# Kernel optimization log

Hardware: AMD Instinct MI355X
Metric: run time of the kernel (lower is better)

The kernel has to match this reference:

```python
import jax, jax.numpy as jnp
import numpy as np

B, N, F_IN = 32, 1024, 64   # batch, num_nodes, diffusion_size[0]
K = 3                        # expansion_step
H = 2                        # num_heads
HID, RAW, OUT, CLS = 128, 128, 128, 2
D1, D2 = 128, 128            # diffusion_size[1], diffusion_size[2]
CAT = D1 + RAW               # concat dim fed to attention (h || h_prime) = 256


def setup_inputs() -> dict:
    key = jax.random.key(0)
    ks = jax.random.split(key, 40)
    g = lambda i, shape: jax.random.normal(ks[i], shape, dtype=jnp.float32) * 0.05
    inp = {
        'X': jax.random.normal(ks[0], (B, N, F_IN), dtype=jnp.float32),
        'A': jax.random.uniform(ks[1], (B, N, N), dtype=jnp.float32),
        # transition tensors / mixing weights (only the 2 layers used in forward)
        'T': g(2, (2, K, N, N)),
        'theta': jnp.full((2, K), 1.0 / K, dtype=jnp.float32),
        # raw feature projection
        'W_raw': g(3, (F_IN, RAW)), 'b_raw': jnp.zeros((RAW,), jnp.float32),
        # diffusion layer linears
        'Wd0': g(4, (F_IN, D1)), 'bd0': jnp.zeros((D1,), jnp.float32),
        'Wd1': g(5, (D1, D2)),   'bd1': jnp.zeros((D2,), jnp.float32),
        # final classifier
        'W_fin': g(6, (OUT, CLS)), 'b_fin': jnp.zeros((CLS,), jnp.float32),
    }
    # two CatMultiAttn blocks: q/k/v projections (CAT->HID), out proj (HID->OUT)
    i = 7
    for l in range(2):
        for nm in ('q', 'k', 'v'):
            inp[f'W{nm}{l}'] = g(i, (CAT, HID)); i += 1
            inp[f'b{nm}{l}'] = jnp.zeros((HID,), jnp.float32)
        inp[f'Wo{l}'] = g(i, (HID, OUT)); i += 1
        inp[f'bo{l}'] = jnp.zeros((OUT,), jnp.float32)
    return inp


def _diffusion(theta_l, T_l, h, A, W, b):
    # Q = sum_k theta_k * T_k  (generalized graph diffusion transition)
    Q = jnp.einsum('k,kij->ij', theta_l, T_l)          # [N,N]
    S = Q[None, :, :] * A                               # [B,N,N] mask by adjacency
    z = jnp.einsum('bij,bjf->bif', S, h)                # diffuse features
    return jax.nn.relu(z @ W + b)


def _cat_attn(h, hp, Wq, bq, Wk, bk, Wv, bv, Wo, bo):
    # concatenate diffused + embedding features, multi-head self-attn over nodes
    x = jnp.concatenate([h, hp], axis=-1)               # [B,N,CAT]
    b, n, _ = x.shape
    q = (x @ Wq + bq).reshape(b, n, H, HID // H)
    k = (x @ Wk + bk).reshape(b, n, H, HID // H)
    v = (x @ Wv + bv).reshape(b, n, H, HID // H)
    scale = jnp.asarray(1.0 / np.sqrt(HID // H), x.dtype)
    s = jnp.einsum('bnhd,bmhd->bhnm', q, k) * scale     # [B,H,N,N]
    p = jax.nn.softmax(s, axis=-1)
    ctx = jnp.einsum('bhnm,bmhd->bnhd', p, v).reshape(b, n, HID)
    return jax.nn.relu(ctx @ Wo + bo)


def reference(X, A, T, theta, W_raw, b_raw, Wd0, bd0, Wd1, bd1,
              W_fin, b_fin,
              Wq0, bq0, Wk0, bk0, Wv0, bv0, Wo0, bo0,
              Wq1, bq1, Wk1, bk1, Wv1, bv1, Wo1, bo1):
    theta_soft = jax.nn.softmax(theta, axis=-1)         # [2,K]
    h_prime = X @ W_raw + b_raw                          # [B,N,RAW]
    # layer 0
    h = _diffusion(theta_soft[0], T[0], X, A, Wd0, bd0)  # [B,N,D1]
    h_prime = _cat_attn(h, h_prime, Wq0, bq0, Wk0, bk0, Wv0, bv0, Wo0, bo0)
    # layer 1 (residual fusion)
    h = _diffusion(theta_soft[1], T[1], h, A, Wd1, bd1)  # [B,N,D2]
    h_prime = h_prime + _cat_attn(h, h_prime, Wq1, bq1, Wk1, bk1, Wv1, bv1, Wo1, bo1)
    return h_prime @ W_fin + b_fin                       # [B,N,CLS]
```

## Files before the change

kernel.cpp:

```cpp
#include <hip/hip_runtime.h>
#include <hip/hip_bf16.h>

typedef __hip_bfloat16 bf16;
typedef __attribute__((ext_vector_type(8))) short s8b;
typedef __attribute__((ext_vector_type(4))) short s4b;
typedef __attribute__((ext_vector_type(4))) float f4;

#define BB   32
#define NN   1024
#define FIN  64
#define HEADS 2
#define DH   64
#define HIDD 128
#define SZQ  ((size_t)BB * NN * HIDD)

__device__ __forceinline__ ushort f2bf(float x) {
    bf16 h = __float2bfloat16(x);
    return *(ushort*)&h;
}
__device__ __forceinline__ float bfbits2f(ushort h) {
    union { uint u; float f; } c; c.u = (uint)h << 16; return c.f;
}
__device__ __forceinline__ uint pk_bf16(float lo, float hi) {
    return (uint)f2bf(lo) | ((uint)f2bf(hi) << 16);
}
union U8 { short s[8]; s8b v; };
union U4 { short s[4]; s4b v; };
union UQ { ushort u[8]; s8b v; };

__global__ __launch_bounds__(256) void setup_kernel(
        const float* __restrict__ raw, const float* __restrict__ d0,
        const float* __restrict__ d1,
        const float* __restrict__ q0w, const float* __restrict__ k0w,
        const float* __restrict__ v0w, const float* __restrict__ o0w,
        const float* __restrict__ q1w, const float* __restrict__ k1w,
        const float* __restrict__ v1w, const float* __restrict__ o1w,
        ushort* __restrict__ Whi, ushort* __restrict__ Wlo,
        const float* __restrict__ T, const float* __restrict__ theta,
        ushort* __restrict__ Q0hi, ushort* __restrict__ Q0lo,
        ushort* __restrict__ Q1hi, ushort* __restrict__ Q1lo,
        const float* __restrict__ X,
        ushort* __restrict__ XT_hi, ushort* __restrict__ XT_lo) {
    __shared__ float tile[64][65];
    const int bid = blockIdx.x;
    const int t = threadIdx.x;
    if (bid < 1024) {
        int id = bid * 256 + t;
        const float* src; int K, off;
        if      (id <   8192) { src = raw; K =  64; off = 0; }
        else if (id <  16384) { src = d0;  K =  64; off = 8192; }
        else if (id <  32768) { src = d1;  K = 128; off = 16384; }
        else if (id <  65536) { src = q0w; K = 256; off = 32768; }
        else if (id <  98304) { src = k0w; K = 256; off = 65536; }
        else if (id < 131072) { src = v0w; K = 256; off = 98304; }
        else if (id < 147456) { src = o0w; K = 128; off = 131072; }
        else if (id < 180224) { src = q1w; K = 256; off = 147456; }
        else if (id < 212992) { src = k1w; K = 256; off = 180224; }
        else if (id < 245760) { src = v1w; K = 256; off = 212992; }
        else                  { src = o1w; K = 128; off = 245760; }
        int il = id - off;
        int k = il >> 7, c = il & 127;
        float w = src[il];
        ushort h = f2bf(w);
        Whi[off + c * K + k] = h;
        Wlo[off + c * K + k] = f2bf(w - bfbits2f(h));
    } else if (bid < 1536) {
        const int tb = bid - 1024;
        const int b  = tb >> 4;
        const int n0 = (tb & 15) * 64;
        {
            int nl = t >> 2, f0 = (t & 3) * 16;
            const float* xp = X + ((size_t)b * NN + n0 + nl) * 64 + f0;
#pragma unroll
            for (int i = 0; i < 16; i += 4)
                *(float4*)&tile[nl][f0 + i] = *(const float4*)(xp + i);
        }
        __syncthreads();
        {
            int f = t >> 2, n1 = (t & 3) * 16;
            U8 h0, h1, l0, l1;
#pragma unroll
            for (int i = 0; i < 16; i++) {
                float v = tile[n1 + i][f];
                ushort hh = f2bf(v);
                ushort ll = f2bf(v - bfbits2f(hh));
                if (i < 8) { h0.s[i] = (short)hh; l0.s[i] = (short)ll; }
                else       { h1.s[i - 8] = (short)hh; l1.s[i - 8] = (short)ll; }
            }
            size_t gb = ((size_t)b * 64 + f) * NN + n0 + n1;
            *(s8b*)&XT_hi[gb]     = h0.v;  *(s8b*)&XT_hi[gb + 8] = h1.v;
            *(s8b*)&XT_lo[gb]     = l0.v;  *(s8b*)&XT_lo[gb + 8] = l1.v;
        }
    } else {
        const int layer = (bid < 2048) ? 0 : 1;
        ushort* Qhi = layer ? Q1hi : Q0hi;
        ushort* Qlo = layer ? Q1lo : Q0lo;
        float t0 = theta[layer * 3 + 0];
        float t1 = theta[layer * 3 + 1];
        float t2 = theta[layer * 3 + 2];
        float m  = fmaxf(t0, fmaxf(t1, t2));
        float e0 = expf(t0 - m), e1 = expf(t1 - m), e2 = expf(t2 - m);
        float inv = 1.0f / (e0 + e1 + e2);
        e0 *= inv; e1 *= inv; e2 *= inv;
        size_t base = ((size_t)((bid - 1536) & 511) * 256 + t) * 8;
        const float* Tl = T + (size_t)layer * 3 * NN * NN;
        U8 hi, lo;
#pragma unroll
        for (int i = 0; i < 8; i++) {
            float q = e0 * Tl[base + i]
                    + e1 * Tl[base + i + (size_t)NN * NN]
                    + e2 * Tl[base + i + (size_t)2 * NN * NN];
            ushort hh = f2bf(q);
            hi.s[i] = (short)hh;
            lo.s[i] = (short)f2bf(q - bfbits2f(hh));
        }
        *(s8b*)&Qhi[base] = hi.v;
        *(s8b*)&Qlo[base] = lo.v;
    }
}

template<int F, bool WRITE_HT>
__global__ __launch_bounds__(512, 4) void diff_dense_kernel(
        const ushort* __restrict__ Qhi, const ushort* __restrict__ Qlo,
        const float* __restrict__ A,
        const ushort* __restrict__ hT_hi, const ushort* __restrict__ hT_lo,
        const ushort* __restrict__ WT_hi, const ushort* __restrict__ WT_lo,
        const float* __restrict__ bias,
        float* __restrict__ hout,
        ushort* __restrict__ hiT, ushort* __restrict__ loT) {
    constexpr int SS  = 72;
    constexpr int NT  = F / 16;
    constexpr int NCW = NT / 4;
    constexpr int SZ2 = F + 8;
    constexpr int P1 = 2 * 64 * SS + 2 * F * SS;
    constexpr int P2 = 2 * 64 * SZ2 + 2 * 128 * 40;
    __shared__ short smem[(P1 > P2) ? P1 : P2];
    short* Shi = smem;
    short* Slo = Shi + 64 * SS;
    short* Hhi = Slo + 64 * SS;
    short* Hlo = Hhi + (size_t)F * SS;
    short* Zhi = smem;
    short* Zlo = Zhi + 64 * SZ2;
    short* Wsh = Zlo + 64 * SZ2;
    short* Wsl = Wsh + 128 * 40;

    const int bidx = blockIdx.x;
    const int u  = bidx >> 3;
    const int b  = (bidx & 7) + 8 * (u >> 4);
    const int i0 = (u & 15) * 64;
    const int t  = threadIdx.x;
    const int w  = t >> 6, lane = t & 63;
    const int quad = lane >> 4, c = lane & 15;
    const int rh = w >> 2;
    const int ch = w & 3;

    const int srow = t >> 3, scol = (t & 7) * 8;
    const float*  Ap = A   + ((size_t)b * NN + i0 + srow) * NN + scol;
    const ushort* Qh = Qhi + (size_t)(i0 + srow) * NN + scol;
    const ushort* Ql = Qlo + (size_t)(i0 + srow) * NN + scol;
    constexpr int HTR = 512 / F;
    constexpr int HJ  = 64 / HTR;
    constexpr int HV  = HJ / 8;
    const int hrow = t / HTR, hcol = (t % HTR) * HJ;
    const ushort* Hh = hT_hi + ((size_t)b * F + hrow) * NN + hcol;
    const ushort* Hl = hT_lo + ((size_t)b * F + hrow) * NN + hcol;

    f4 acc[2][NCW];
#pragma unroll
    for (int st = 0; st < 2; st++)
#pragma unroll
        for (int i = 0; i < NCW; i++) acc[st][i] = (f4){0.f, 0.f, 0.f, 0.f};

    float4 a0 = *(const float4*)Ap, a1 = *(const float4*)(Ap + 4);
    s8b hhv[HV], hlv[HV];
#pragma unroll
    for (int vv = 0; vv < HV; vv++) {
        hhv[vv] = *(const s8b*)(Hh + 8 * vv);
        hlv[vv] = *(const s8b*)(Hl + 8 * vv);
    }
    UQ qh, ql;
    qh.v = *(const s8b*)Qh;
    ql.v = *(const s8b*)Ql;

#pragma unroll 1
    for (int j0 = 0; j0 < NN; j0 += 64) {
        __syncthreads();
        {
            float av[8] = {a0.x, a0.y, a0.z, a0.w, a1.x, a1.y, a1.z, a1.w};
            U8 hi, lo;
#pragma unroll
            for (int i = 0; i < 8; i++) {
                float q = bfbits2f(qh.u[i]) + bfbits2f(ql.u[i]);
                float s = q * av[i];
                ushort hb = f2bf(s);
                hi.s[i] = (short)hb;
                lo.s[i] = (short)f2bf(s - bfbits2f(hb));
            }
            *(s8b*)&Shi[srow * SS + scol] = hi.v;
            *(s8b*)&Slo[srow * SS + scol] = lo.v;
#pragma unroll
            for (int vv = 0; vv < HV; vv++) {
                *(s8b*)&Hhi[hrow * SS + hcol + 8 * vv] = hhv[vv];
                *(s8b*)&Hlo[hrow * SS + hcol + 8 * vv] = hlv[vv];
            }
        }
        __syncthreads();

        if (j0 + 64 < NN) {
            a0 = *(const float4*)(Ap + j0 + 64);
            a1 = *(const float4*)(Ap + j0 + 68);
#pragma unroll
            for (int vv = 0; vv < HV; vv++) {
                hhv[vv] = *(const s8b*)(Hh + j0 + 64 + 8 * vv);
                hlv[vv] = *(const s8b*)(Hl + j0 + 64 + 8 * vv);
            }
            qh.v = *(const s8b*)(Qh + j0 + 64);
            ql.v = *(const s8b*)(Ql + j0 + 64);
        }

#pragma unroll
        for (int ks = 0; ks < 2; ks++) {
            s8b ah0 = *(const s8b*)&Shi[(32 * rh + c) * SS + ks * 32 + quad * 8];
            s8b al0 = *(const s8b*)&Slo[(32 * rh + c) * SS + ks * 32 + quad * 8];
            s8b ah1 = *(const s8b*)&Shi[(32 * rh + 16 + c) * SS + ks * 32 + quad * 8];
            s8b al1 = *(const s8b*)&Slo[(32 * rh + 16 + c) * SS + ks * 32 + quad * 8];
#pragma unroll
            for (int ctn = 0; ctn < NCW; ctn++) {
                const int nt = ch * NCW + ctn;
                s8b bhi = *(const s8b*)&Hhi[(nt * 16 + c) * SS + ks * 32 + quad * 8];
                s8b blo = *(const s8b*)&Hlo[(nt * 16 + c) * SS + ks * 32 + quad * 8];
                acc[0][ctn] = __builtin_amdgcn_mfma_f32_16x16x32_bf16(ah0, bhi, acc[0][ctn], 0, 0, 0);
                acc[0][ctn] = __builtin_amdgcn_mfma_f32_16x16x32_bf16(al0, bhi, acc[0][ctn], 0, 0, 0);
                acc[0][ctn] = __builtin_amdgcn_mfma_f32_16x16x32_bf16(ah0, blo, acc[0][ctn], 0, 0, 0);
                acc[1][ctn] = __builtin_amdgcn_mfma_f32_16x16x32_bf16(ah1, bhi, acc[1][ctn], 0, 0, 0);
                acc[1][ctn] = __builtin_amdgcn_mfma_f32_16x16x32_bf16(al1, bhi, acc[1][ctn], 0, 0, 0);
                acc[1][ctn] = __builtin_amdgcn_mfma_f32_16x16x32_bf16(ah1, blo, acc[1][ctn], 0, 0, 0);
            }
        }
    }

    __syncthreads();
#pragma unroll
    for (int st = 0; st < 2; st++)
#pragma unroll
        for (int ctn = 0; ctn < NCW; ctn++)
#pragma unroll
            for (int r = 0; r < 4; r++) {
                const int row = 32 * rh + 16 * st + quad * 4 + r;
                const int col = (ch * NCW + ctn) * 16 + c;
                float v = acc[st][ctn][r];
                ushort hh = f2bf(v);
                Zhi[row * SZ2 + col] = (short)hh;
                Zlo[row * SZ2 + col] = (short)f2bf(v - bfbits2f(hh));
            }

    const int rh2 = w >> 2;
    const int ch2 = w & 3;
    f4 acc2[2][2];
#pragma unroll
    for (int st = 0; st < 2; st++)
#pragma unroll
        for (int i = 0; i < 2; i++) acc2[st][i] = (f4){0.f, 0.f, 0.f, 0.f};

    constexpr int NKT = F / 32;
    const int wcc = t >> 2, wkk = (t & 3) * 8;
    s8b pwh = *(const s8b*)&WT_hi[(size_t)wcc * F + wkk];
    s8b pwl = *(const s8b*)&WT_lo[(size_t)wcc * F + wkk];
    for (int kt = 0; kt < NKT; kt++) {
        __syncthreads();
        *(s8b*)&Wsh[wcc * 40 + wkk] = pwh;
        *(s8b*)&Wsl[wcc * 40 + wkk] = pwl;
        __syncthreads();
        if (kt + 1 < NKT) {
            size_t gsrc = (size_t)wcc * F + (kt + 1) * 32 + wkk;
            pwh = *(const s8b*)&WT_hi[gsrc];
            pwl = *(const s8b*)&WT_lo[gsrc];
        }

        s8b ah0 = *(const s8b*)&Zhi[(32 * rh2 + c) * SZ2 + kt * 32 + quad * 8];
        s8b al0 = *(const s8b*)&Zlo[(32 * rh2 + c) * SZ2 + kt * 32 + quad * 8];
        s8b ah1 = *(const s8b*)&Zhi[(32 * rh2 + 16 + c) * SZ2 + kt * 32 + quad * 8];
        s8b al1 = *(const s8b*)&Zlo[(32 * rh2 + 16 + c) * SZ2 + kt * 32 + quad * 8];
#pragma unroll
        for (int ct = 0; ct < 2; ct++) {
            s8b bh = *(const s8b*)&Wsh[(ch2 * 32 + ct * 16 + c) * 40 + quad * 8];
            s8b bl = *(const s8b*)&Wsl[(ch2 * 32 + ct * 16 + c) * 40 + quad * 8];
            acc2[0][ct] = __builtin_amdgcn_mfma_f32_16x16x32_bf16(ah0, bh, acc2[0][ct], 0, 0, 0);
            acc2[0][ct] = __builtin_amdgcn_mfma_f32_16x16x32_bf16(al0, bh, acc2[0][ct], 0, 0, 0);
            acc2[0][ct] = __builtin_amdgcn_mfma_f32_16x16x32_bf16(ah0, bl, acc2[0][ct], 0, 0, 0);
            acc2[1][ct] = __builtin_amdgcn_mfma_f32_16x16x32_bf16(ah1, bh, acc2[1][ct], 0, 0, 0);
            acc2[1][ct] = __builtin_amdgcn_mfma_f32_16x16x32_bf16(al1, bh, acc2[1][ct], 0, 0, 0);
            acc2[1][ct] = __builtin_amdgcn_mfma_f32_16x16x32_bf16(ah1, bl, acc2[1][ct], 0, 0, 0);
        }
    }

#pragma unroll
    for (int st = 0; st < 2; st++) {
        const int rg0 = i0 + 32 * rh2 + 16 * st + quad * 4;
#pragma unroll
        for (int ct = 0; ct < 2; ct++) {
            const int col = ch2 * 32 + ct * 16 + c;
            float bv = bias[col];
            float vv[4];
#pragma unroll
            for (int r = 0; r < 4; r++) {
                float v = fmaxf(acc2[st][ct][r] + bv, 0.f);
                hout[((size_t)b * NN + rg0 + r) * 128 + col] = v;
                vv[r] = v;
            }
            if (WRITE_HT) {
                U4 ph, pl;
#pragma unroll
                for (int r = 0; r < 4; r++) {
                    ushort hh = f2bf(vv[r]);
                    ph.s[r] = (short)hh;
                    pl.s[r] = (short)f2bf(vv[r] - bfbits2f(hh));
                }
                size_t tb = ((size_t)b * 128 + col) * NN + rg0;
                *(s4b*)&hiT[tb] = ph.v;
                *(s4b*)&loT[tb] = pl.v;
            }
        }
    }
}

template<int K1, int K2, int CB, bool RELU, bool RESID, int OMODE>
__global__ __launch_bounds__(512) void dense_mfma_kernel(
        const float* __restrict__ in1, const float* __restrict__ in2,
        const ushort* __restrict__ WT_hi, const ushort* __restrict__ WT_lo,
        const float* __restrict__ bias, const float* __restrict__ biask,
        const float* __restrict__ biasv,
        float* __restrict__ out, ushort* __restrict__ outq) {
    constexpr int KD  = K1 + K2;
    constexpr int NKT = KD / 32;
    constexpr int NCH = CB / 32;
    constexpr int WCH = CB * 4;
    constexpr int WPT = (WCH + 511) / 512;
    __shared__ short Xhi[128][40], Xlo[128][40];
    __shared__ short Whi[CB][40], Wlo[CB][40];

    int bx, by;
    if (OMODE == 1) {
        const int xcd = blockIdx.x & 7, qq = blockIdx.x >> 3;
        by = qq & 1;
        bx = ((qq >> 1) << 3) | xcd;
    } else { bx = blockIdx.x; by = blockIdx.y; }
    const int r0 = bx * 128;
    const int c0 = by * CB;
    const int t  = threadIdx.x;
    const int w  = t >> 6, lane = t & 63;
    const int quad = lane >> 4, c = lane & 15;
    const int rh = w >> 1;
    const int ch = w & 1;

    f4 acc[2][NCH];
#pragma unroll
    for (int st = 0; st < 2; st++)
#pragma unroll
        for (int i = 0; i < NCH; i++) acc[st][i] = (f4){0.f, 0.f, 0.f, 0.f};

    const int xrow = t >> 2, xkk = (t & 3) * 8;
    float4 pa, pbq;
    s8b pwh[WPT], pwl[WPT];
    auto loadX = [&](int k0) {
        int g = r0 + xrow;
        const float* p;
        if (K2 > 0) {
            int k = k0 + xkk;
            p = (k < K1) ? (in1 + (size_t)g * K1 + k)
                         : (in2 + (size_t)g * K2 + (k - K1));
        } else {
            p = in1 + (size_t)g * K1 + k0 + xkk;
        }
        pa = *(const float4*)p; pbq = *(const float4*)(p + 4);
    };
    auto loadW = [&](int k0) {
#pragma unroll
        for (int i = 0; i < WPT; i++) {
            int id = t + i * 512;
            if ((WCH % 512 == 0) || id < WCH) {
                int cc = id >> 2, kk = (id & 3) * 8;
                size_t gsrc = (size_t)(c0 + cc) * KD + k0 + kk;
                pwh[i] = *(const s8b*)&WT_hi[gsrc];
                pwl[i] = *(const s8b*)&WT_lo[gsrc];
            }
        }
    };
    loadX(0); loadW(0);

    for (int kt = 0; kt < NKT; kt++) {
        __syncthreads();
        {
            float sv[8] = {pa.x, pa.y, pa.z, pa.w, pbq.x, pbq.y, pbq.z, pbq.w};
            U8 hi, lo;
#pragma unroll
            for (int i = 0; i < 8; i++) {
                ushort hh = f2bf(sv[i]);
                hi.s[i] = (short)hh;
                lo.s[i] = (short)f2bf(sv[i] - bfbits2f(hh));
            }
            *(s8b*)&Xhi[xrow][xkk] = hi.v;
            *(s8b*)&Xlo[xrow][xkk] = lo.v;
        }
        {
#pragma unroll
            for (int i = 0; i < WPT; i++) {
                int id = t + i * 512;
                if ((WCH % 512 == 0) || id < WCH) {
                    int cc = id >> 2, kk = (id & 3) * 8;
                    *(s8b*)&Whi[cc][kk] = pwh[i];
                    *(s8b*)&Wlo[cc][kk] = pwl[i];
                }
            }
        }
        __syncthreads();
        if (kt + 1 < NKT) { loadX(kt * 32 + 32); loadW(kt * 32 + 32); }

        s8b ah0 = *(const s8b*)&Xhi[32 * rh + c][quad * 8];
        s8b al0 = *(const s8b*)&Xlo[32 * rh + c][quad * 8];
        s8b ah1 = *(const s8b*)&Xhi[32 * rh + 16 + c][quad * 8];
        s8b al1 = *(const s8b*)&Xlo[32 * rh + 16 + c][quad * 8];
#pragma unroll
        for (int ct = 0; ct < NCH; ct++) {
            s8b bh = *(const s8b*)&Whi[ch * (CB / 2) + ct * 16 + c][quad * 8];
            s8b bl = *(const s8b*)&Wlo[ch * (CB / 2) + ct * 16 + c][quad * 8];
            acc[0][ct] = __builtin_amdgcn_mfma_f32_16x16x32_bf16(ah0, bh, acc[0][ct], 0, 0, 0);
            acc[0][ct] = __builtin_amdgcn_mfma_f32_16x16x32_bf16(al0, bh, acc[0][ct], 0, 0, 0);
            acc[0][ct] = __builtin_amdgcn_mfma_f32_16x16x32_bf16(ah0, bl, acc[0][ct], 0, 0, 0);
            acc[1][ct] = __builtin_amdgcn_mfma_f32_16x16x32_bf16(ah1, bh, acc[1][ct], 0, 0, 0);
            acc[1][ct] = __builtin_amdgcn_mfma_f32_16x16x32_bf16(al1, bh, acc[1][ct], 0, 0, 0);
            acc[1][ct] = __builtin_amdgcn_mfma_f32_16x16x32_bf16(ah1, bl, acc[1][ct], 0, 0, 0);
        }
    }

#pragma unroll
    for (int st = 0; st < 2; st++) {
        const int row_g0 = r0 + 32 * rh + 16 * st + quad * 4;
#pragma unroll
        for (int ct = 0; ct < NCH; ct++) {
            const int col = c0 + ch * (CB / 2) + ct * 16 + c;
            if (OMODE == 1) {
                int tensor = col >> 7, cc2 = col & 127;
                float bv = (tensor == 0 ? bias : tensor == 1 ? biask : biasv)[cc2];
                int head = cc2 >> 6, d = cc2 & 63;
                int b = row_g0 >> 10, n = row_g0 & 1023;
                if (tensor == 2) {
                    U4 pk;
#pragma unroll
                    for (int r = 0; r < 4; r++) pk.s[r] = (short)f2bf(acc[st][ct][r] + bv);
                    size_t addr = (((size_t)b * HEADS + head) * 64 + d) * NN + n;
                    *(s4b*)&outq[2 * SZQ + addr] = pk.v;
                } else {
                    ushort* dst = outq + (size_t)tensor * SZQ
                                + (((size_t)b * HEADS + head) * NN + n) * 64 + d;
#pragma unroll
                    for (int r = 0; r < 4; r++) dst[(size_t)r * 64] = f2bf(acc[st][ct][r] + bv);
                }
            } else {
                float bv = bias[col];
#pragma unroll
                for (int r = 0; r < 4; r++) {
                    float v = acc[st][ct][r] + bv;
                    if (RELU) v = fmaxf(v, 0.f);
                    size_t o = (size_t)(row_g0 + r) * 128 + col;
                    if (RESID) v += out[o];
                    out[o] = v;
                }
            }
        }
    }
}

template<bool FINAL>
__global__ __launch_bounds__(512) void attn_oproj_kernel(
        const ushort* __restrict__ q, const ushort* __restrict__ k,
        const ushort* __restrict__ vt,
        const ushort* __restrict__ WoT_hi, const ushort* __restrict__ WoT_lo,
        const float* __restrict__ bo,
        float* __restrict__ hp,
        const float* __restrict__ Wfin, const float* __restrict__ bfin,
        float* __restrict__ fout) {
    constexpr int ZS = 136;
    constexpr int PB = 2 * 128 * ZS + 2 * 128 * 40 + 512;
    __shared__ short smem[PB];
    short* Ks  = smem;
    short* Vt  = smem + 128 * 72;
    short* Zhi = smem;
    short* Zlo = Zhi + 128 * ZS;
    short* Wsh = Zlo + 128 * ZS;
    short* Wsl = Wsh + 128 * 40;
    float* red = (float*)(Wsl + 128 * 40);

    const int bidx = blockIdx.x;
    const int u  = bidx >> 3;
    const int b  = (bidx & 7) + 8 * (u >> 3);
    const int n0 = (u & 7) * 128;
    const int t  = threadIdx.x;
    const int w  = t >> 6;
    const int lane = t & 63;
    const int quad = lane >> 4, c = lane & 15;
    const float scale = 0.125f;

    const int skey = t >> 2, sd0 = (t & 3) * 16;
    const int svd  = t >> 3, svc = (t & 7) * 16;

    s8b pk0, pk1, pv0, pv1;
    auto loadKV = [&](size_t base, int kt0) {
        const ushort* kr = k + base + (size_t)(kt0 + skey) * 64 + sd0;
        pk0 = *(const s8b*)kr;
        pk1 = *(const s8b*)(kr + 8);
        const ushort* vr = vt + base + (size_t)svd * NN + kt0 + svc;
        pv0 = *(const s8b*)vr;
        pv1 = *(const s8b*)(vr + 8);
    };

    f4 Oh[2][4];
    float li[2];

#pragma unroll
    for (int h = 0; h < 2; h++) {
        const size_t kvbase = ((size_t)(b * HEADS + h)) * NN * 64;
        s8b qf0, qf1;
        {
            const ushort* qrow = q + kvbase + (size_t)(n0 + 16 * w + c) * 64;
            qf0 = *(const s8b*)(qrow + quad * 8);
            qf1 = *(const s8b*)(qrow + 32 + quad * 8);
        }
        if (h == 0) loadKV(kvbase, 0);
        f4 O[4];
#pragma unroll
        for (int i = 0; i < 4; i++) O[i] = (f4){0.f, 0.f, 0.f, 0.f};
        float l_i = 0.f;

        for (int kt0 = 0; kt0 < NN; kt0 += 128) {
            __syncthreads();
            {
                *(s8b*)&Ks[skey * 72 + sd0]     = pk0;
                *(s8b*)&Ks[skey * 72 + sd0 + 8] = pk1;
                *(s8b*)&Vt[svd * 136 + svc]     = pv0;
                *(s8b*)&Vt[svd * 136 + svc + 8] = pv1;
            }
            __syncthreads();
            if (kt0 + 128 < NN)      loadKV(kvbase, kt0 + 128);
            else if (h == 0)         loadKV(kvbase + (size_t)NN * 64, 0);

            f4 sg[4][2];
#pragma unroll
            for (int g = 0; g < 4; g++) {
                const int kb = g * 32;
                sg[g][0] = (f4){0.f, 0.f, 0.f, 0.f};
                sg[g][1] = (f4){0.f, 0.f, 0.f, 0.f};
#pragma unroll
                for (int ck = 0; ck < 2; ck++) {
                    s8b ka = *(const s8b*)&Ks[(kb + c) * 72 + ck * 32 + quad * 8];
                    s8b kB = *(const s8b*)&Ks[(kb + 16 + c) * 72 + ck * 32 + quad * 8];
                    s8b qf = ck ? qf1 : qf0;
                    sg[g][0] = __builtin_amdgcn_mfma_f32_16x16x32_bf16(ka, qf, sg[g][0], 0, 0, 0);
                    sg[g][1] = __builtin_amdgcn_mfma_f32_16x16x32_bf16(kB, qf, sg[g][1], 0, 0, 0);
                }
            }
            float pv[4][8];
            float ps = 0.f;
#pragma unroll
            for (int g = 0; g < 4; g++)
#pragma unroll
                for (int r = 0; r < 4; r++) {
                    pv[g][r]     = __expf(sg[g][0][r] * scale);
                    pv[g][4 + r] = __expf(sg[g][1][r] * scale);
                    ps += pv[g][r] + pv[g][4 + r];
                }
            ps += __shfl_xor(ps, 16);
            ps += __shfl_xor(ps, 32);
            l_i += ps;

            int addr0 = ((((2 * quad) & 3) << 4) | c) << 2;
            int addr1 = ((((2 * quad + 1) & 3) << 4) | c) << 2;
            int tsel = quad >> 1;
#pragma unroll
            for (int g = 0; g < 4; g++) {
                const int kb = g * 32;
                uint Da01 = pk_bf16(pv[g][0], pv[g][1]), Da23 = pk_bf16(pv[g][2], pv[g][3]);
                uint Db01 = pk_bf16(pv[g][4], pv[g][5]), Db23 = pk_bf16(pv[g][6], pv[g][7]);
                int A01_0 = __builtin_amdgcn_ds_bpermute(addr0, (int)Da01);
                int A23_0 = __builtin_amdgcn_ds_bpermute(addr0, (int)Da23);
                int B01_0 = __builtin_amdgcn_ds_bpermute(addr0, (int)Db01);
                int B23_0 = __builtin_amdgcn_ds_bpermute(addr0, (int)Db23);
                int A01_1 = __builtin_amdgcn_ds_bpermute(addr1, (int)Da01);
                int A23_1 = __builtin_amdgcn_ds_bpermute(addr1, (int)Da23);
                int B01_1 = __builtin_amdgcn_ds_bpermute(addr1, (int)Db01);
                int B23_1 = __builtin_amdgcn_ds_bpermute(addr1, (int)Db23);
                union { int i[4]; s8b s; } pf;
                pf.i[0] = tsel ? B01_0 : A01_0;
                pf.i[1] = tsel ? B23_0 : A23_0;
                pf.i[2] = tsel ? B01_1 : A01_1;
                pf.i[3] = tsel ? B23_1 : A23_1;
#pragma unroll
                for (int dt = 0; dt < 4; dt++) {
                    s8b vf = *(const s8b*)&Vt[(16 * dt + c) * 136 + kb + quad * 8];
                    O[dt] = __builtin_amdgcn_mfma_f32_16x16x32_bf16(vf, pf.s, O[dt], 0, 0, 0);
                }
            }
        }
        li[h] = 1.0f / l_i;
#pragma unroll
        for (int dt = 0; dt < 4; dt++) Oh[h][dt] = O[dt];
    }

    __syncthreads();
    {
        const int zrow = 16 * w + c;
#pragma unroll
        for (int h = 0; h < 2; h++) {
            float inv = li[h];
#pragma unroll
            for (int dt = 0; dt < 4; dt++) {
                U4 ph, pl;
#pragma unroll
                for (int r = 0; r < 4; r++) {
                    float v = Oh[h][dt][r] * inv;
                    ushort hh = f2bf(v);
                    ph.s[r] = (short)hh;
                    pl.s[r] = (short)f2bf(v - bfbits2f(hh));
                }
                int col = h * 64 + 16 * dt + 4 * quad;
                *(s4b*)&Zhi[zrow * ZS + col] = ph.v;
                *(s4b*)&Zlo[zrow * ZS + col] = pl.v;
            }
        }
    }

    const int rh = w >> 1;
    const int ch = w & 1;
    f4 acc[2][4];
#pragma unroll
    for (int st = 0; st < 2; st++)
#pragma unroll
        for (int i = 0; i < 4; i++) acc[st][i] = (f4){0.f, 0.f, 0.f, 0.f};

    const int occ = t >> 2, okk = (t & 3) * 8;
    s8b owh = *(const s8b*)&WoT_hi[(size_t)occ * 128 + okk];
    s8b owl = *(const s8b*)&WoT_lo[(size_t)occ * 128 + okk];
    for (int kt = 0; kt < 4; kt++) {
        __syncthreads();
        *(s8b*)&Wsh[occ * 40 + okk] = owh;
        *(s8b*)&Wsl[occ * 40 + okk] = owl;
        __syncthreads();
        if (kt + 1 < 4) {
            size_t gsrc = (size_t)occ * 128 + (kt + 1) * 32 + okk;
            owh = *(const s8b*)&WoT_hi[gsrc];
            owl = *(const s8b*)&WoT_lo[gsrc];
        }

        s8b ah0 = *(const s8b*)&Zhi[(32 * rh + c) * ZS + kt * 32 + quad * 8];
        s8b al0 = *(const s8b*)&Zlo[(32 * rh + c) * ZS + kt * 32 + quad * 8];
        s8b ah1 = *(const s8b*)&Zhi[(32 * rh + 16 + c) * ZS + kt * 32 + quad * 8];
        s8b al1 = *(const s8b*)&Zlo[(32 * rh + 16 + c) * ZS + kt * 32 + quad * 8];
#pragma unroll
        for (int ct = 0; ct < 4; ct++) {
            s8b bh = *(const s8b*)&Wsh[(ch * 64 + ct * 16 + c) * 40 + quad * 8];
            s8b bl = *(const s8b*)&Wsl[(ch * 64 + ct * 16 + c) * 40 + quad * 8];
            acc[0][ct] = __builtin_amdgcn_mfma_f32_16x16x32_bf16(ah0, bh, acc[0][ct], 0, 0, 0);
            acc[0][ct] = __builtin_amdgcn_mfma_f32_16x16x32_bf16(al0, bh, acc[0][ct], 0, 0, 0);
            acc[0][ct] = __builtin_amdgcn_mfma_f32_16x16x32_bf16(ah0, bl, acc[0][ct], 0, 0, 0);
            acc[1][ct] = __builtin_amdgcn_mfma_f32_16x16x32_bf16(ah1, bh, acc[1][ct], 0, 0, 0);
            acc[1][ct] = __builtin_amdgcn_mfma_f32_16x16x32_bf16(al1, bh, acc[1][ct], 0, 0, 0);
            acc[1][ct] = __builtin_amdgcn_mfma_f32_16x16x32_bf16(ah1, bl, acc[1][ct], 0, 0, 0);
        }
    }

    if (FINAL) {
        float fc[2][2][4];
#pragma unroll
        for (int st = 0; st < 2; st++)
#pragma unroll
            for (int o = 0; o < 2; o++)
#pragma unroll
                for (int r = 0; r < 4; r++) fc[st][o][r] = 0.f;
#pragma unroll
        for (int ct = 0; ct < 4; ct++) {
            const int col = ch * 64 + ct * 16 + c;
            float bv = bo[col];
            float w0 = Wfin[col * 2], w1 = Wfin[col * 2 + 1];
#pragma unroll
            for (int st = 0; st < 2; st++) {
                const size_t rg = (size_t)b * NN + n0 + 32 * rh + 16 * st + quad * 4;
#pragma unroll
                for (int r = 0; r < 4; r++) {
                    float v = fmaxf(acc[st][ct][r] + bv, 0.f);
                    v += hp[(rg + r) * 128 + col];
                    fc[st][0][r] += v * w0;
                    fc[st][1][r] += v * w1;
                }
            }
        }
#pragma unroll
        for (int st = 0; st < 2; st++)
#pragma unroll
            for (int r = 0; r < 4; r++) {
                float a0 = fc[st][0][r], a1 = fc[st][1][r];
#pragma unroll
                for (int off = 1; off < 16; off <<= 1) {
                    a0 += __shfl_xor(a0, off, 16);
                    a1 += __shfl_xor(a1, off, 16);
                }
                fc[st][0][r] = a0; fc[st][1][r] = a1;
            }
        if (ch == 1 && c == 0) {
#pragma unroll
            for (int st = 0; st < 2; st++)
#pragma unroll
                for (int r = 0; r < 4; r++) {
                    int lr = 32 * rh + 16 * st + quad * 4 + r;
                    red[lr * 2]     = fc[st][0][r];
                    red[lr * 2 + 1] = fc[st][1][r];
                }
        }
        __syncthreads();
        if (ch == 0 && c == 0) {
#pragma unroll
            for (int st = 0; st < 2; st++)
#pragma unroll
                for (int r = 0; r < 4; r++) {
                    int lr = 32 * rh + 16 * st + quad * 4 + r;
                    size_t row = (size_t)b * NN + n0 + lr;
                    fout[row * 2]     = fc[st][0][r] + red[lr * 2]     + bfin[0];
                    fout[row * 2 + 1] = fc[st][1][r] + red[lr * 2 + 1] + bfin[1];
                }
        }
        return;
    }

#pragma unroll
    for (int st = 0; st < 2; st++) {
        const size_t rg = (size_t)b * NN + n0 + 32 * rh + 16 * st + quad * 4;
#pragma unroll
        for (int ct = 0; ct < 4; ct++) {
            const int col = ch * 64 + ct * 16 + c;
            float bv = bo[col];
#pragma unroll
            for (int r = 0; r < 4; r++)
                hp[(rg + r) * 128 + col] = fmaxf(acc[st][ct][r] + bv, 0.f);
        }
    }
}

extern "C" void kernel_launch(void* const* d_in, const int* in_sizes, int n_in,
                              void* d_out, int out_size, void* d_ws, size_t ws_size,
                              hipStream_t stream) {
    (void)in_sizes; (void)n_in; (void)out_size; (void)ws_size;
    const float* X     = (const float*)d_in[0];
    const float* A     = (const float*)d_in[1];
    const float* T     = (const float*)d_in[2];
    const float* theta = (const float*)d_in[3];
    const float* W_raw = (const float*)d_in[4];
    const float* b_raw = (const float*)d_in[5];
    const float* Wd0   = (const float*)d_in[6];
    const float* bd0   = (const float*)d_in[7];
    const float* Wd1   = (const float*)d_in[8];
    const float* bd1   = (const float*)d_in[9];
    const float* W_fin = (const float*)d_in[10];
    const float* b_fin = (const float*)d_in[11];
    const float* Wq0 = (const float*)d_in[12]; const float* bq0 = (const float*)d_in[13];
    const float* Wk0 = (const float*)d_in[14]; const float* bk0 = (const float*)d_in[15];
    const float* Wv0 = (const float*)d_in[16]; const float* bv0 = (const float*)d_in[17];
    const float* Wo0 = (const float*)d_in[18]; const float* bo0 = (const float*)d_in[19];
    const float* Wq1 = (const float*)d_in[20]; const float* bq1 = (const float*)d_in[21];
    const float* Wk1 = (const float*)d_in[22]; const float* bk1 = (const float*)d_in[23];
    const float* Wv1 = (const float*)d_in[24]; const float* bv1 = (const float*)d_in[25];
    const float* Wo1 = (const float*)d_in[26]; const float* bo1 = (const float*)d_in[27];

    float* ws   = (float*)d_ws;
    const size_t SZ = (size_t)BB * NN * HIDD;
    ushort* Q0hi = (ushort*)ws;
    ushort* Q0lo = Q0hi + (size_t)NN * NN;
    float* hp   = ws + (size_t)NN * NN;
    float* h    = hp + SZ;
    float* z    = h + SZ;
    ushort* qb  = (ushort*)(z + SZ);
    ushort* kb  = qb + SZ;
    ushort* XT_hi = qb + 3 * SZ;
    ushort* XT_lo = XT_hi + SZ / 2;
    ushort* hT_hi = XT_lo + SZ / 2;
    ushort* hT_lo = hT_hi + SZ;
    ushort* WT_hi = hT_lo + SZ;
    ushort* WT_lo = WT_hi + 262144;
    ushort* Q1hi = WT_lo + 262144;
    ushort* Q1lo = Q1hi + (size_t)NN * NN;

    const int OFF_RAW = 0, OFF_D0 = 8192, OFF_D1 = 16384, OFF_QKV0 = 32768,
              OFF_O0 = 131072, OFF_QKV1 = 147456, OFF_O1 = 245760;

    const int attnGrid = BB * (NN / 128);
    const int diffGrid = BB * (NN / 64);
    const dim3 dg1(256, 1);

    setup_kernel<<<2560, 256, 0, stream>>>(W_raw, Wd0, Wd1, Wq0, Wk0, Wv0, Wo0,
                                           Wq1, Wk1, Wv1, Wo1, WT_hi, WT_lo,
                                           T, theta, Q0hi, Q0lo, Q1hi, Q1lo,
                                           X, XT_hi, XT_lo);

    dense_mfma_kernel<64, 0, 128, false, false, 0><<<dg1, 512, 0, stream>>>(
        X, nullptr, WT_hi + OFF_RAW, WT_lo + OFF_RAW, b_raw, nullptr, nullptr,
        hp, nullptr);
    diff_dense_kernel<64, true><<<diffGrid, 512, 0, stream>>>(
        Q0hi, Q0lo, A, XT_hi, XT_lo, WT_hi + OFF_D0, WT_lo + OFF_D0, bd0,
        h, hT_hi, hT_lo);
    dense_mfma_kernel<128, 128, 192, false, false, 1><<<512, 512, 0, stream>>>(
        h, hp, WT_hi + OFF_QKV0, WT_lo + OFF_QKV0, bq0, bk0, bv0,
        nullptr, qb);
    attn_oproj_kernel<false><<<attnGrid, 512, 0, stream>>>(
        qb, kb, qb + 2 * SZ, WT_hi + OFF_O0, WT_lo + OFF_O0, bo0,
        hp, nullptr, nullptr, nullptr);

    diff_dense_kernel<128, false><<<diffGrid, 512, 0, stream>>>(
        Q1hi, Q1lo, A, hT_hi, hT_lo, WT_hi + OFF_D1, WT_lo + OFF_D1, bd1,
        h, nullptr, nullptr);
    dense_mfma_kernel<128, 128, 192, false, false, 1><<<512, 512, 0, stream>>>(
        h, hp, WT_hi + OFF_QKV1, WT_lo + OFF_QKV1, bq1, bk1, bv1,
        nullptr, qb);
    attn_oproj_kernel<true><<<attnGrid, 512, 0, stream>>>(
        qb, kb, qb + 2 * SZ, WT_hi + OFF_O1, WT_lo + OFF_O1, bo1,
        hp, W_fin, b_fin, (float*)d_out);
}
```

Before: 490.5 us.

## Merge independent diffusion and dense GEMM kernels into shared multi-role launches

Turns the diffusion and dense GEMM kernels into device bodies that take a shared smem pointer and a block index. Independent stages now run together in one launch with interleaved block roles: layer-0 diffusion with the raw projection, and layer-1 diffusion with the layer-0 QKV projection, which only depends on layer-0 outputs. Layer-1 diffusion now writes to a separate h2 buffer so it can run alongside the QKV read of h. The aim is fewer launches and filling the GPU with concurrent independent work. The cost is lost per-kernel launch bounds (occupancy hint 4 dropped), a larger shared allocation for the smaller role, and mixed role workloads inside one grid.

```diff
diff --git a/kernel.cpp b/kernel.cpp
--- a/kernel.cpp
+++ b/kernel.cpp
@@ -120,7 +120,8 @@
 }
 
 template<int F, bool WRITE_HT>
-__global__ __launch_bounds__(512, 4) void diff_dense_kernel(
+__device__ __forceinline__ void diff_dense_body(
+        short* smem, int bidx,
         const ushort* __restrict__ Qhi, const ushort* __restrict__ Qlo,
         const float* __restrict__ A,
         const ushort* __restrict__ hT_hi, const ushort* __restrict__ hT_lo,
@@ -132,9 +133,6 @@
     constexpr int NT  = F / 16;
     constexpr int NCW = NT / 4;
     constexpr int SZ2 = F + 8;
-    constexpr int P1 = 2 * 64 * SS + 2 * F * SS;
-    constexpr int P2 = 2 * 64 * SZ2 + 2 * 128 * 40;
-    __shared__ short smem[(P1 > P2) ? P1 : P2];
     short* Shi = smem;
     short* Slo = Shi + 64 * SS;
     short* Hhi = Slo + 64 * SS;
@@ -144,7 +142,6 @@
     short* Wsh = Zlo + 64 * SZ2;
     short* Wsl = Wsh + 128 * 40;
 
-    const int bidx = blockIdx.x;
     const int u  = bidx >> 3;
     const int b  = (bidx & 7) + 8 * (u >> 4);
     const int i0 = (u & 15) * 64;
@@ -167,9 +164,9 @@
 
     f4 acc[2][NCW];
 #pragma unroll
-    for (int st = 0; st < 2; st++)
-#pragma unroll
-        for (int i = 0; i < NCW; i++) acc[st][i] = (f4){0.f, 0.f, 0.f, 0.f};
+    for (int i = 0; i < 2; i++)
+#pragma unroll
+        for (int j = 0; j < NCW; j++) acc[i][j] = (f4){0.f, 0.f, 0.f, 0.f};
 
     float4 a0 = *(const float4*)Ap, a1 = *(const float4*)(Ap + 4);
     s8b hhv[HV], hlv[HV];
@@ -325,7 +322,8 @@
 }
 
 template<int K1, int K2, int CB, bool RELU, bool RESID, int OMODE>
-__global__ __launch_bounds__(512) void dense_mfma_kernel(
+__device__ __forceinline__ void dense_body(
+        short* smem, int bidx,
         const float* __restrict__ in1, const float* __restrict__ in2,
         const ushort* __restrict__ WT_hi, const ushort* __restrict__ WT_lo,
         const float* __restrict__ bias, const float* __restrict__ biask,
@@ -336,15 +334,17 @@
     constexpr int NCH = CB / 32;
     constexpr int WCH = CB * 4;
     constexpr int WPT = (WCH + 511) / 512;
-    __shared__ short Xhi[128][40], Xlo[128][40];
-    __shared__ short Whi[CB][40], Wlo[CB][40];
+    short* Xhi = smem;
+    short* Xlo = Xhi + 128 * 40;
+    short* Whi = Xlo + 128 * 40;
+    short* Wlo = Whi + CB * 40;
 
     int bx, by;
     if (OMODE == 1) {
-        const int xcd = blockIdx.x & 7, qq = blockIdx.x >> 3;
+        const int xcd = bidx & 7, qq = bidx >> 3;
         by = qq & 1;
         bx = ((qq >> 1) << 3) | xcd;
-    } else { bx = blockIdx.x; by = blockIdx.y; }
+    } else { bx = bidx; by = 0; }
     const int r0 = bx * 128;
     const int c0 = by * CB;
     const int t  = threadIdx.x;
@@ -399,8 +399,8 @@
                 hi.s[i] = (short)hh;
                 lo.s[i] = (short)f2bf(sv[i] - bfbits2f(hh));
             }
-            *(s8b*)&Xhi[xrow][xkk] = hi.v;
-            *(s8b*)&Xlo[xrow][xkk] = lo.v;
+            *(s8b*)&Xhi[xrow * 40 + xkk] = hi.v;
+            *(s8b*)&Xlo[xrow * 40 + xkk] = lo.v;
         }
         {
 #pragma unroll
@@ -408,22 +408,22 @@
                 int id = t + i * 512;
                 if ((WCH % 512 == 0) || id < WCH) {
                     int cc = id >> 2, kk = (id & 3) * 8;
-                    *(s8b*)&Whi[cc][kk] = pwh[i];
-                    *(s8b*)&Wlo[cc][kk] = pwl[i];
+                    *(s8b*)&Whi[cc * 40 + kk] = pwh[i];
+                    *(s8b*)&Wlo[cc * 40 + kk] = pwl[i];
                 }
             }
         }
         __syncthreads();
         if (kt + 1 < NKT) { loadX(kt * 32 + 32); loadW(kt * 32 + 32); }
 
-        s8b ah0 = *(const s8b*)&Xhi[32 * rh + c][quad * 8];
-        s8b al0 = *(const s8b*)&Xlo[32 * rh + c][quad * 8];
-        s8b ah1 = *(const s8b*)&Xhi[32 * rh + 16 + c][quad * 8];
-        s8b al1 = *(const s8b*)&Xlo[32 * rh + 16 + c][quad * 8];
+        s8b ah0 = *(const s8b*)&Xhi[(32 * rh + c) * 40 + quad * 8];
+        s8b al0 = *(const s8b*)&Xlo[(32 * rh + c) * 40 + quad * 8];
+        s8b ah1 = *(const s8b*)&Xhi[(32 * rh + 16 + c) * 40 + quad * 8];
+        s8b al1 = *(const s8b*)&Xlo[(32 * rh + 16 + c) * 40 + quad * 8];
 #pragma unroll
         for (int ct = 0; ct < NCH; ct++) {
-            s8b bh = *(const s8b*)&Whi[ch * (CB / 2) + ct * 16 + c][quad * 8];
-            s8b bl = *(const s8b*)&Wlo[ch * (CB / 2) + ct * 16 + c][quad * 8];
+            s8b bh = *(const s8b*)&Whi[(ch * (CB / 2) + ct * 16 + c) * 40 + quad * 8];
+            s8b bl = *(const s8b*)&Wlo[(ch * (CB / 2) + ct * 16 + c) * 40 + quad * 8];
             acc[0][ct] = __builtin_amdgcn_mfma_f32_16x16x32_bf16(ah0, bh, acc[0][ct], 0, 0, 0);
             acc[0][ct] = __builtin_amdgcn_mfma_f32_16x16x32_bf16(al0, bh, acc[0][ct], 0, 0, 0);
             acc[0][ct] = __builtin_amdgcn_mfma_f32_16x16x32_bf16(ah0, bl, acc[0][ct], 0, 0, 0);
@@ -469,6 +469,62 @@
             }
         }
     }
+}
+
+__global__ __launch_bounds__(512) void m1_kernel(
+        const ushort* __restrict__ Q0hi, const ushort* __restrict__ Q0lo,
+        const float* __restrict__ A,
+        const ushort* __restrict__ XT_hi, const ushort* __restrict__ XT_lo,
+        const ushort* __restrict__ WTd0_hi, const ushort* __restrict__ WTd0_lo,
+        const float* __restrict__ bd0, float* __restrict__ h,
+        ushort* __restrict__ hT_hi, ushort* __restrict__ hT_lo,
+        const float* __restrict__ X,
+        const ushort* __restrict__ WTraw_hi, const ushort* __restrict__ WTraw_lo,
+        const float* __restrict__ b_raw, float* __restrict__ hp) {
+    __shared__ short smem[20480];
+    const int bidx = blockIdx.x;
+    const int r = bidx % 3, g = bidx / 3;
+    if (r < 2) {
+        diff_dense_body<64, true>(smem, g * 2 + r, Q0hi, Q0lo, A, XT_hi, XT_lo,
+                                  WTd0_hi, WTd0_lo, bd0, h, hT_hi, hT_lo);
+    } else {
+        dense_body<64, 0, 128, false, false, 0>(smem, g, X, nullptr,
+                                                WTraw_hi, WTraw_lo, b_raw,
+                                                nullptr, nullptr, hp, nullptr);
+    }
+}
+
+__global__ __launch_bounds__(512) void m2_kernel(
+        const ushort* __restrict__ Q1hi, const ushort* __restrict__ Q1lo,
+        const float* __restrict__ A,
+        const ushort* __restrict__ hT_hi, const ushort* __restrict__ hT_lo,
+        const ushort* __restrict__ WTd1_hi, const ushort* __restrict__ WTd1_lo,
+        const float* __restrict__ bd1, float* __restrict__ h2,
+        const float* __restrict__ h, const float* __restrict__ hp,
+        const ushort* __restrict__ WTq_hi, const ushort* __restrict__ WTq_lo,
+        const float* __restrict__ bq, const float* __restrict__ bk,
+        const float* __restrict__ bv, ushort* __restrict__ qb) {
+    __shared__ short smem[27648];
+    const int bidx = blockIdx.x;
+    if ((bidx & 1) == 0) {
+        diff_dense_body<128, false>(smem, bidx >> 1, Q1hi, Q1lo, A, hT_hi, hT_lo,
+                                    WTd1_hi, WTd1_lo, bd1, h2, nullptr, nullptr);
+    } else {
+        dense_body<128, 128, 192, false, false, 1>(smem, bidx >> 1, h, hp,
+                                                   WTq_hi, WTq_lo, bq, bk, bv,
+                                                   nullptr, qb);
+    }
+}
+
+__global__ __launch_bounds__(512) void qkv_kernel(
+        const float* __restrict__ in1, const float* __restrict__ in2,
+        const ushort* __restrict__ WT_hi, const ushort* __restrict__ WT_lo,
+        const float* __restrict__ bias, const float* __restrict__ biask,
+        const float* __restrict__ biasv, ushort* __restrict__ outq) {
+    __shared__ short smem[25600];
+    dense_body<128, 128, 192, false, false, 1>(smem, blockIdx.x, in1, in2,
+                                               WT_hi, WT_lo, bias, biask, biasv,
+                                               nullptr, outq);
 }
 
 template<bool FINAL>
@@ -775,8 +831,8 @@
     ushort* Q0lo = Q0hi + (size_t)NN * NN;
     float* hp   = ws + (size_t)NN * NN;
     float* h    = hp + SZ;
-    float* z    = h + SZ;
-    ushort* qb  = (ushort*)(z + SZ);
+    float* h2   = h + SZ;
+    ushort* qb  = (ushort*)(h2 + SZ);
     ushort* kb  = qb + SZ;
     ushort* XT_hi = qb + 3 * SZ;
     ushort* XT_lo = XT_hi + SZ / 2;
@@ -791,33 +847,28 @@
               OFF_O0 = 131072, OFF_QKV1 = 147456, OFF_O1 = 245760;
 
     const int attnGrid = BB * (NN / 128);
-    const int diffGrid = BB * (NN / 64);
-    const dim3 dg1(256, 1);
 
     setup_kernel<<<2560, 256, 0, stream>>>(W_raw, Wd0, Wd1, Wq0, Wk0, Wv0, Wo0,
                                            Wq1, Wk1, Wv1, Wo1, WT_hi, WT_lo,
                                            T, theta, Q0hi, Q0lo, Q1hi, Q1lo,
                                            X, XT_hi, XT_lo);
 
-    dense_mfma_kernel<64, 0, 128, false, false, 0><<<dg1, 512, 0, stream>>>(
-        X, nullptr, WT_hi + OFF_RAW, WT_lo + OFF_RAW, b_raw, nullptr, nullptr,
-        hp, nullptr);
-    diff_dense_kernel<64, true><<<diffGrid, 512, 0, stream>>>(
+    m1_kernel<<<768, 512, 0, stream>>>(
         Q0hi, Q0lo, A, XT_hi, XT_lo, WT_hi + OFF_D0, WT_lo + OFF_D0, bd0,
-        h, hT_hi, hT_lo);
-    dense_mfma_kernel<128, 128, 192, false, false, 1><<<512, 512, 0, stream>>>(
-        h, hp, WT_hi + OFF_QKV0, WT_lo + OFF_QKV0, bq0, bk0, bv0,
-        nullptr, qb);
+        h, hT_hi, hT_lo,
+        X, WT_hi + OFF_RAW, WT_lo + OFF_RAW, b_raw, hp);
+
+    m2_kernel<<<1024, 512, 0, stream>>>(
+        Q1hi, Q1lo, A, hT_hi, hT_lo, WT_hi + OFF_D1, WT_lo + OFF_D1, bd1, h2,
+        h, hp, WT_hi + OFF_QKV0, WT_lo + OFF_QKV0, bq0, bk0, bv0, qb);
+
     attn_oproj_kernel<false><<<attnGrid, 512, 0, stream>>>(
         qb, kb, qb + 2 * SZ, WT_hi + OFF_O0, WT_lo + OFF_O0, bo0,
         hp, nullptr, nullptr, nullptr);
 
-    diff_dense_kernel<128, false><<<diffGrid, 512, 0, stream>>>(
-        Q1hi, Q1lo, A, hT_hi, hT_lo, WT_hi + OFF_D1, WT_lo + OFF_D1, bd1,
-        h, nullptr, nullptr);
-    dense_mfma_kernel<128, 128, 192, false, false, 1><<<512, 512, 0, stream>>>(
-        h, hp, WT_hi + OFF_QKV1, WT_lo + OFF_QKV1, bq1, bk1, bv1,
-        nullptr, qb);
+    qkv_kernel<<<512, 512, 0, stream>>>(
+        h2, hp, WT_hi + OFF_QKV1, WT_lo + OFF_QKV1, bq1, bk1, bv1, qb);
+
     attn_oproj_kernel<true><<<attnGrid, 512, 0, stream>>>(
         qb, kb, qb + 2 * SZ, WT_hi + OFF_O1, WT_lo + OFF_O1, bo1,
         hp, W_fin, b_fin, (float*)d_out);
```

Measured after the change: 492.9 us. About the same (+0.5%).
